# Optimization experiments

Hardware: AMD Instinct MI355X
Metric: run time of the kernel (lower is better)

## Reference

```python
import jax, jax.numpy as jnp
import numpy as np

B, C, H, W = 16, 512, 32, 32
COND_C, L_COND = 768, 77
N_GROUPS, N_HEADS = 8, 8
HEAD = C // N_HEADS
EPS = 1e-5


def setup_inputs() -> dict:
    key = jax.random.key(0)
    ks = jax.random.split(key, 6)
    s = lambda fan_in: 1.0 / np.sqrt(fan_in)
    return {
        "x_0": jax.random.normal(ks[0], (B, C, H, W), jnp.float32),
        "cond": jax.random.normal(ks[1], (B, L_COND, COND_C), jnp.float32),
        "gn_gamma": jnp.ones((C,), jnp.float32),
        "gn_beta": jnp.zeros((C,), jnp.float32),
        "qkv_w": jax.random.normal(ks[2], (3 * C, C), jnp.float32) * s(C),
        "qkv_b": jnp.zeros((3 * C,), jnp.float32),
        "cond_kv_w": jax.random.normal(ks[3], (2 * C, COND_C), jnp.float32) * s(COND_C),
        "cond_kv_b": jnp.zeros((2 * C,), jnp.float32),
        "out_w": jax.random.normal(ks[4], (C, C), jnp.float32) * s(C),
        "out_b": jnp.zeros((C,), jnp.float32),
    }


def reference(x_0, cond, gn_gamma, gn_beta, qkv_w, qkv_b, cond_kv_w, cond_kv_b, out_w, out_b):
    b, c, h, w = x_0.shape
    L = h * w
    # --- GroupNorm over (C/G, H, W) per group, per-channel affine ---
    xg = x_0.reshape(b, N_GROUPS, c // N_GROUPS, h * w)
    mu = xg.mean(axis=(2, 3), keepdims=True)
    var = xg.var(axis=(2, 3), keepdims=True)
    xn = ((xg - mu) * jax.lax.rsqrt(var + EPS)).reshape(b, c, h, w)
    xn = xn * gn_gamma[None, :, None, None] + gn_beta[None, :, None, None]
    # --- to tokens [B, L, C] ---
    x = xn.transpose(0, 2, 3, 1).reshape(b, L, c)
    # --- QKV ---
    qkv = x @ qkv_w.T + qkv_b  # [B, L, 3C]
    q, k, v = jnp.split(qkv, 3, axis=-1)
    q = q.reshape(b, L, N_HEADS, HEAD)
    k = k.reshape(b, L, N_HEADS, HEAD)
    v = v.reshape(b, L, N_HEADS, HEAD)
    # --- conditional K/V ---
    kv_c = cond @ cond_kv_w.T + cond_kv_b  # [B, Lc, 2C]
    k_c, v_c = jnp.split(kv_c, 2, axis=-1)
    Lc = cond.shape[1]
    k_c = k_c.reshape(b, Lc, N_HEADS, HEAD)
    v_c = v_c.reshape(b, Lc, N_HEADS, HEAD)
    K = jnp.concatenate([k, k_c], axis=1)  # [B, L+Lc, H, D]
    V = jnp.concatenate([v, v_c], axis=1)
    # --- attention (full score matrix, as in the original) ---
    scale = HEAD ** -0.5
    scores = jnp.einsum("bqhd,bkhd->bhqk", q, K) * scale
    att = jax.nn.softmax(scores, axis=-1)
    out = jnp.einsum("bhqk,bkhd->bqhd", att, V).reshape(b, L, c)
    out = out @ out_w.T + out_b
    # --- back to image + residual ---
    out = out.reshape(b, h, w, c).transpose(0, 3, 1, 2)
    return out + x_0
```

## Files before the change

### kernel.cpp

```cpp
#include <hip/hip_runtime.h>

typedef short bf16x8 __attribute__((ext_vector_type(8)));
typedef float f32x4 __attribute__((ext_vector_type(4)));
typedef float f32x16 __attribute__((ext_vector_type(16)));
typedef unsigned int u32x4 __attribute__((ext_vector_type(4)));

#define KVP 1152

__device__ __forceinline__ unsigned short f2b(float f) {
    unsigned int u = __float_as_uint(f);
    u += 0x7FFFu + ((u >> 16) & 1u);
    return (unsigned short)(u >> 16);
}

__device__ __forceinline__ f32x4 mfma16(bf16x8 a, bf16x8 b, f32x4 c) {
    return __builtin_amdgcn_mfma_f32_16x16x32_bf16(a, b, c, 0, 0, 0);
}
__device__ __forceinline__ f32x16 mfma32(bf16x8 a, bf16x8 b, f32x16 c) {
    return __builtin_amdgcn_mfma_f32_32x32x16_bf16(a, b, c, 0, 0, 0);
}
__device__ __forceinline__ float exp2_raw(float x) {
    float r; asm("v_exp_f32 %0, %1" : "=v"(r) : "v"(x)); return r;
}
__device__ __forceinline__ unsigned cvt_pk(float lo, float hi) {
    unsigned r; asm("v_cvt_pk_bf16_f32 %0, %1, %2" : "=v"(r) : "v"(lo), "v"(hi)); return r;
}

typedef __attribute__((address_space(3))) unsigned int lds_u32_t;
typedef const __attribute__((address_space(1))) unsigned int glb_u32_t;
__device__ __forceinline__ void async_cp16(const void* g, void* l) {
    __builtin_amdgcn_global_load_lds((glb_u32_t*)(unsigned long long)g,
                                     (lds_u32_t*)(unsigned int)(unsigned long long)l,
                                     16, 0, 0);
}

__global__ __launch_bounds__(256) void gn_part_k(const float* __restrict__ x, float2* __restrict__ part) {
    int blk = blockIdx.x;
    const float4* p = (const float4*)(x + (size_t)blk * 16384);
    float s = 0.f, ss = 0.f;
    for (int i = threadIdx.x; i < 4096; i += 256) {
        float4 v = p[i];
        s  += v.x + v.y + v.z + v.w;
        ss += v.x * v.x + v.y * v.y + v.z * v.z + v.w * v.w;
    }
#pragma unroll
    for (int o = 32; o; o >>= 1) { s += __shfl_down(s, o); ss += __shfl_down(ss, o); }
    __shared__ float red[8];
    int w = threadIdx.x >> 6;
    if ((threadIdx.x & 63) == 0) { red[w] = s; red[4 + w] = ss; }
    __syncthreads();
    if (threadIdx.x == 0) {
        s  = red[0] + red[1] + red[2] + red[3];
        ss = red[4] + red[5] + red[6] + red[7];
        part[blk] = make_float2(s, ss);
    }
}

__global__ __launch_bounds__(256) void gn_apply_k(const float* __restrict__ x, const float2* __restrict__ part,
                                                  const float* __restrict__ gamma, const float* __restrict__ beta,
                                                  unsigned short* __restrict__ xt) {
    int st = blockIdx.x & 15;
    int ct = (blockIdx.x >> 4) & 7;
    int b  = blockIdx.x >> 7;
    int bg = b * 8 + ct;
    float2 p0 = part[4 * bg], p1 = part[4 * bg + 1], p2 = part[4 * bg + 2], p3 = part[4 * bg + 3];
    float s = (p0.x + p1.x) + (p2.x + p3.x);
    float ss = (p0.y + p1.y) + (p2.y + p3.y);
    float mean = s * (1.f / 65536.f);
    float var  = ss * (1.f / 65536.f) - mean * mean;
    float rsig = rsqrtf(var + 1e-5f);
    __shared__ unsigned short tile[64][65];
    int tid = threadIdx.x;
#pragma unroll
    for (int it = 0; it < 4; ++it) {
        int idx = it * 256 + tid;
        int ci = idx >> 4, j4 = idx & 15;
        int c = ct * 64 + ci;
        float4 v = *(const float4*)(x + ((size_t)b * 512 + c) * 1024 + st * 64 + j4 * 4);
        float gs = gamma[c] * rsig;
        float bo = beta[c] - mean * gs;
        tile[j4 * 4 + 0][ci] = f2b(v.x * gs + bo);
        tile[j4 * 4 + 1][ci] = f2b(v.y * gs + bo);
        tile[j4 * 4 + 2][ci] = f2b(v.z * gs + bo);
        tile[j4 * 4 + 3][ci] = f2b(v.w * gs + bo);
    }
    __syncthreads();
#pragma unroll
    for (int it = 0; it < 4; ++it) {
        int idx = it * 256 + tid;
        int si = idx >> 4, q = idx & 15;
        uint2 u;
        u.x = (unsigned)tile[si][q * 4 + 0] | ((unsigned)tile[si][q * 4 + 1] << 16);
        u.y = (unsigned)tile[si][q * 4 + 2] | ((unsigned)tile[si][q * 4 + 3] << 16);
        *(uint2*)(xt + ((size_t)b * 1024 + st * 64 + si) * 512 + ct * 64 + q * 4) = u;
    }
}

__global__ __launch_bounds__(256) void cvt_k(const float* __restrict__ in, unsigned short* __restrict__ out, int n4) {
    int i = blockIdx.x * 256 + threadIdx.x;
    if (i < n4) {
        float4 v = ((const float4*)in)[i];
        uint2 u;
        u.x = (unsigned)f2b(v.x) | ((unsigned)f2b(v.y) << 16);
        u.y = (unsigned)f2b(v.z) | ((unsigned)f2b(v.w) << 16);
        ((uint2*)out)[i] = u;
    }
}

template <int EPI>
__global__ __launch_bounds__(256) void gemm128_k(const unsigned short* __restrict__ A,
                                                 const unsigned short* __restrict__ Bw,
                                                 const float* __restrict__ bias,
                                                 int K,
                                                 unsigned short* __restrict__ Qo,
                                                 unsigned short* __restrict__ Ko,
                                                 unsigned short* __restrict__ Vo,
                                                 const float* __restrict__ x0,
                                                 float* __restrict__ outp) {
    __shared__ __align__(16) unsigned short As[3][4096];
    __shared__ __align__(16) unsigned short Bs[3][4096];
    const int m0 = blockIdx.x * 128, n0 = blockIdx.y * 128;
    const int tid = threadIdx.x, lane = tid & 63, w = tid >> 6;
    const int wr = w >> 1, wc = w & 1;
    const int lc = lane & 15, lg = lane >> 4;

    const int sRow = lane >> 2;
    const int sSlot = (lane & 3) ^ ((lane >> 3) & 3);
    const unsigned short* aSrc0 = A + (size_t)(m0 + 16 * w + sRow) * K + sSlot * 8;
    const unsigned short* aSrc1 = A + (size_t)(m0 + 64 + 16 * w + sRow) * K + sSlot * 8;
    const unsigned short* bSrc0 = Bw + (size_t)(n0 + 16 * w + sRow) * K + sSlot * 8;
    const unsigned short* bSrc1 = Bw + (size_t)(n0 + 64 + 16 * w + sRow) * K + sSlot * 8;

    const int rSlot8 = (lg ^ ((lc >> 1) & 3)) * 8;

    f32x4 acc[4][4];
#pragma unroll
    for (int m = 0; m < 4; ++m)
#pragma unroll
        for (int n = 0; n < 4; ++n) acc[m][n] = (f32x4){0.f, 0.f, 0.f, 0.f};

    const int nT = K >> 5;
    async_cp16(aSrc0, &As[0][w * 512]);
    async_cp16(aSrc1, &As[0][(4 + w) * 512]);
    async_cp16(bSrc0, &Bs[0][w * 512]);
    async_cp16(bSrc1, &Bs[0][(4 + w) * 512]);
    async_cp16(aSrc0 + 32, &As[1][w * 512]);
    async_cp16(aSrc1 + 32, &As[1][(4 + w) * 512]);
    async_cp16(bSrc0 + 32, &Bs[1][w * 512]);
    async_cp16(bSrc1 + 32, &Bs[1][(4 + w) * 512]);

    int c = 0;
#pragma unroll 1
    for (int t = 0; t < nT; ++t) {
        if (t + 2 < nT) {
            int c2 = c + 2; if (c2 >= 3) c2 -= 3;
            const int k2 = (t + 2) << 5;
            async_cp16(aSrc0 + k2, &As[c2][w * 512]);
            async_cp16(aSrc1 + k2, &As[c2][(4 + w) * 512]);
            async_cp16(bSrc0 + k2, &Bs[c2][w * 512]);
            async_cp16(bSrc1 + k2, &Bs[c2][(4 + w) * 512]);
            asm volatile("s_waitcnt vmcnt(8)" ::: "memory");
        } else if (t + 1 < nT) {
            asm volatile("s_waitcnt vmcnt(4)" ::: "memory");
        } else {
            asm volatile("s_waitcnt vmcnt(0)" ::: "memory");
        }
        __builtin_amdgcn_s_barrier();

        bf16x8 af[4], bfr[4];
#pragma unroll
        for (int m = 0; m < 4; ++m)
            af[m] = *(const bf16x8*)&As[c][(wr * 64 + m * 16 + lc) * 32 + rSlot8];
#pragma unroll
        for (int n = 0; n < 4; ++n)
            bfr[n] = *(const bf16x8*)&Bs[c][(wc * 64 + n * 16 + lc) * 32 + rSlot8];
        asm volatile("s_waitcnt lgkmcnt(0)" ::: "memory");
        __builtin_amdgcn_sched_barrier(0);
        __builtin_amdgcn_s_barrier();

#pragma unroll
        for (int m = 0; m < 4; ++m)
#pragma unroll
            for (int n = 0; n < 4; ++n) {
                if (EPI == 0) acc[m][n] = mfma16(bfr[n], af[m], acc[m][n]);
                else          acc[m][n] = mfma16(af[m], bfr[n], acc[m][n]);
            }

        ++c; if (c == 3) c = 0;
    }

    if (EPI == 0) {
        const bool isQ = (n0 < 512);
        const float sc = isQ ? (0.125f * 1.44269504089f) : 1.f;
#pragma unroll
        for (int n = 0; n < 4; ++n) {
            const int c0 = n0 + wc * 64 + n * 16 + lg * 4;
            const float4 b4 = *(const float4*)&bias[c0];
#pragma unroll
            for (int m = 0; m < 4; ++m) {
                const int tok = m0 + wr * 64 + m * 16 + lc;
                const int b = tok >> 10, l = tok & 1023;
                float v0 = (acc[m][n][0] + b4.x) * sc;
                float v1 = (acc[m][n][1] + b4.y) * sc;
                float v2 = (acc[m][n][2] + b4.z) * sc;
                float v3 = (acc[m][n][3] + b4.w) * sc;
                uint2 u = make_uint2(cvt_pk(v0, v1), cvt_pk(v2, v3));
                if (isQ) {
                    const int hh = c0 >> 6, d = c0 & 63;
                    *(uint2*)(Qo + ((size_t)(b * 8 + hh) * 1024 + l) * 64 + d) = u;
                } else {
                    const int hh = (c0 - 512) >> 6, d = c0 & 63;
                    *(uint2*)(Ko + ((size_t)(b * 8 + hh) * KVP + l) * 64 + d) = u;
                }
            }
        }
    } else if (EPI == 1) {
#pragma unroll
        for (int n = 0; n < 4; ++n) {
            const int j = n0 + wc * 64 + n * 16 + lc;
            const int hh = j >> 6, d = j & 63;
            const float bv = bias[j];
#pragma unroll
            for (int m = 0; m < 4; ++m) {
                const int t0 = m0 + wr * 64 + m * 16 + lg * 4;
                const int b = t0 >> 10, l0 = t0 & 1023;
                uint2 u = make_uint2(cvt_pk(acc[m][n][0] + bv, acc[m][n][1] + bv),
                                     cvt_pk(acc[m][n][2] + bv, acc[m][n][3] + bv));
                *(uint2*)(Vo + ((size_t)(b * 8 + hh) * 64 + d) * KVP + l0) = u;
            }
        }
    } else {
#pragma unroll
        for (int n = 0; n < 4; ++n) {
            const int col = n0 + wc * 64 + n * 16 + lc;
            const float bv = bias[col];
#pragma unroll
            for (int m = 0; m < 4; ++m) {
                const int t0 = m0 + wr * 64 + m * 16 + lg * 4;
                const size_t a = ((size_t)(t0 >> 10) * 512 + col) * 1024 + (t0 & 1023);
                float4 xv = *(const float4*)(x0 + a);
                float4 o;
                o.x = acc[m][n][0] + bv + xv.x;
                o.y = acc[m][n][1] + bv + xv.y;
                o.z = acc[m][n][2] + bv + xv.z;
                o.w = acc[m][n][3] + bv + xv.w;
                *(float4*)(outp + a) = o;
            }
        }
    }
}

__global__ __launch_bounds__(256) void gemm_nt_k(const unsigned short* __restrict__ A,
                                                 const unsigned short* __restrict__ Bw,
                                                 const float* __restrict__ bias,
                                                 int M, int N, int K,
                                                 unsigned short* __restrict__ Ko,
                                                 unsigned short* __restrict__ Vo) {
    __shared__ unsigned short As[64][40];
    __shared__ unsigned short Bs[64][40];
    const int m0 = blockIdx.x * 64, n0 = blockIdx.y * 64;
    const int tid = threadIdx.x, lane = tid & 63, w = tid >> 6;
    const int lc = lane & 15, lg = lane >> 4;
    const int lrow = tid >> 2, lseg = tid & 3;
    f32x4 acc[4];
#pragma unroll
    for (int i = 0; i < 4; ++i) acc[i] = (f32x4){0.f, 0.f, 0.f, 0.f};

    for (int k0 = 0; k0 < K; k0 += 32) {
        uint4 av = make_uint4(0u, 0u, 0u, 0u);
        if (m0 + lrow < M) av = *(const uint4*)(A + (size_t)(m0 + lrow) * K + k0 + lseg * 8);
        *(uint4*)&As[lrow][lseg * 8] = av;
        uint4 bv = *(const uint4*)(Bw + (size_t)(n0 + lrow) * K + k0 + lseg * 8);
        *(uint4*)&Bs[lrow][lseg * 8] = bv;
        __syncthreads();
        bf16x8 af = *(const bf16x8*)&As[w * 16 + lc][lg * 8];
#pragma unroll
        for (int ct = 0; ct < 4; ++ct) {
            bf16x8 bfr = *(const bf16x8*)&Bs[ct * 16 + lc][lg * 8];
            acc[ct] = mfma16(af, bfr, acc[ct]);
        }
        __syncthreads();
    }

    const int rbase = m0 + w * 16 + lg * 4;
#pragma unroll
    for (int ct = 0; ct < 4; ++ct) {
        int col = n0 + ct * 16 + lc;
        float bv = bias[col];
#pragma unroll
        for (int r = 0; r < 4; ++r) {
            int token = rbase + r;
            if (token >= M) continue;
            float val = acc[ct][r] + bv;
            int b = token / 77, l = token - b * 77;
            if (col < 512) {
                int hh = col >> 6, d = col & 63;
                Ko[((size_t)(b * 8 + hh) * KVP + 1024 + l) * 64 + d] = f2b(val);
            } else {
                int j = col - 512, hh = j >> 6, d = j & 63;
                Vo[((size_t)(b * 8 + hh) * 64 + d) * KVP + 1024 + l] = f2b(val);
            }
        }
    }
}

__global__ __launch_bounds__(512) void attn2_k(const unsigned short* __restrict__ Q,
                                               const unsigned short* __restrict__ Kb,
                                               const unsigned short* __restrict__ Vt,
                                               unsigned short* __restrict__ atok) {
    __shared__ __align__(16) unsigned short lds[18432];

    const int bh = blockIdx.x >> 2;
    const int qt = blockIdx.x & 3;
    const int w  = threadIdx.x >> 6;
    const int lane = threadIdx.x & 63;
    const int ql = lane & 31, hi = lane >> 5;
    const int q0 = qt * 256 + w * 32;

    bf16x8 qf[4];
    const unsigned short* Qp = Q + ((size_t)bh * 1024 + q0 + ql) * 64 + hi * 8;
#pragma unroll
    for (int ks = 0; ks < 4; ++ks) qf[ks] = *(const bf16x8*)(Qp + ks * 16);

    const unsigned short* Kg = Kb + (size_t)bh * KVP * 64;
    const unsigned short* Vg = Vt + (size_t)bh * 64 * KVP;

    const int srow = lane >> 3;
    const int sc   = (((lane & 7) ^ (lane >> 3)) << 3);

    f32x16 o0, o1;
#pragma unroll
    for (int i = 0; i < 16; ++i) { o0[i] = 0.f; o1[i] = 0.f; }
    float mreg = -1e30f, lsum = 0.f;

    {
        uint4 kr = *(const uint4*)(Kg + (size_t)(8 * w + srow) * 64 + sc);
        uint4 vr = *(const uint4*)(Vg + (size_t)(8 * w + srow) * KVP + sc);
        *(uint4*)&lds[w * 512 + lane * 8] = kr;
        *(uint4*)&lds[4096 + w * 512 + lane * 8] = vr;
    }
    __syncthreads();

    int cur = 0;
    for (int it = 0; it < 18; ++it) {
        const int kv0 = it * 64;
        const bool pre = (it < 17);
        uint4 kn, vn;
        if (pre) {
            kn = *(const uint4*)(Kg + (size_t)(kv0 + 64 + 8 * w + srow) * 64 + sc);
            vn = *(const uint4*)(Vg + (size_t)(8 * w + srow) * KVP + kv0 + 64 + sc);
        }
        const int kb = cur * 8192, vb = cur * 8192 + 4096;

        f32x16 s0, s1;
#pragma unroll
        for (int i = 0; i < 16; ++i) { s0[i] = 0.f; s1[i] = 0.f; }
#pragma unroll
        for (int ks = 0; ks < 4; ++ks) {
            const int sl = ((ks * 2 + hi) ^ (ql & 7)) << 3;
            bf16x8 kf0 = *(const bf16x8*)&lds[kb + ql * 64 + sl];
            bf16x8 kf1 = *(const bf16x8*)&lds[kb + (32 + ql) * 64 + sl];
            s0 = mfma32(kf0, qf[ks], s0);
            s1 = mfma32(kf1, qf[ks], s1);
        }
        if (kv0 == 1088) {
#pragma unroll
            for (int r = 0; r < 16; ++r) {
                int kva = 1088 + (r & 3) + 8 * (r >> 2) + 4 * hi;
                if (kva >= 1101) s0[r] = -1e30f;
                if (kva + 32 >= 1101) s1[r] = -1e30f;
            }
        }

        float t[16];
#pragma unroll
        for (int i = 0; i < 16; ++i) t[i] = fmaxf(s0[i], s1[i]);
#pragma unroll
        for (int st = 8; st; st >>= 1)
#pragma unroll
            for (int i = 0; i < st; ++i) t[i] = fmaxf(t[i], t[i + st]);
        float pmax = fmaxf(t[0], __shfl_xor(t[0], 32));

        if (__any(pmax > mreg + 8.f)) {
            float mn = fmaxf(mreg, pmax);
            float al = exp2_raw(mreg - mn);
            mreg = mn;
            lsum *= al;
#pragma unroll
            for (int i = 0; i < 16; ++i) { o0[i] *= al; o1[i] *= al; }
        }

        unsigned pk0[8], pk1[8];
        float sA = 0.f, sB = 0.f, sC = 0.f, sD = 0.f;
#pragma unroll
        for (int i = 0; i < 8; ++i) {
            float a0 = exp2_raw(s0[2 * i] - mreg), a1 = exp2_raw(s0[2 * i + 1] - mreg);
            float b0 = exp2_raw(s1[2 * i] - mreg), b1 = exp2_raw(s1[2 * i + 1] - mreg);
            pk0[i] = cvt_pk(a0, a1);
            pk1[i] = cvt_pk(b0, b1);
            sA += a0; sB += a1; sC += b0; sD += b1;
        }
        float ls = (sA + sB) + (sC + sD);
        ls += __shfl_xor(ls, 32);
        lsum += ls;

#pragma unroll
        for (int t2 = 0; t2 < 2; ++t2) {
            const unsigned* pk = t2 ? pk1 : pk0;
#pragma unroll
            for (int v = 0; v < 2; ++v) {
                unsigned a0 = pk[4 * v], a1 = pk[4 * v + 1], a2 = pk[4 * v + 2], a3 = pk[4 * v + 3];
                unsigned x = __shfl_xor(hi ? a0 : a2, 32);
                unsigned y = __shfl_xor(hi ? a1 : a3, 32);
                u32x4 fw;
                fw.x = hi ? x : a0; fw.y = hi ? y : a1; fw.z = hi ? a2 : x; fw.w = hi ? a3 : y;
                bf16x8 pf = __builtin_bit_cast(bf16x8, fw);
                const int ks2 = 2 * t2 + v;
                const int sl = ((ks2 * 2 + hi) ^ (ql & 7)) << 3;
                bf16x8 vf0 = *(const bf16x8*)&lds[vb + ql * 64 + sl];
                bf16x8 vf1 = *(const bf16x8*)&lds[vb + (32 + ql) * 64 + sl];
                o0 = mfma32(vf0, pf, o0);
                o1 = mfma32(vf1, pf, o1);
            }
        }

        if (pre) {
            *(uint4*)&lds[(cur ^ 1) * 8192 + w * 512 + lane * 8] = kn;
            *(uint4*)&lds[(cur ^ 1) * 8192 + 4096 + w * 512 + lane * 8] = vn;
        }
        __syncthreads();
        cur ^= 1;
    }

    float rinv = 1.f / lsum;
    unsigned short* sw = &lds[w * 2304];
#pragma unroll
    for (int dt = 0; dt < 2; ++dt) {
#pragma unroll
        for (int rp = 0; rp < 8; ++rp) {
            float e0 = (dt ? o1[2 * rp] : o0[2 * rp]) * rinv;
            float e1 = (dt ? o1[2 * rp + 1] : o0[2 * rp + 1]) * rinv;
            int d = dt * 32 + ((2 * rp) & 3) + 8 * ((2 * rp) >> 2) + 4 * hi;
            *(unsigned*)&sw[ql * 72 + d] = cvt_pk(e0, e1);
        }
    }
    __syncthreads();
    {
        int i = threadIdx.x >> 1, hf = threadIdx.x & 1;
        const unsigned short* src = &lds[(i >> 5) * 2304 + (i & 31) * 72 + hf * 32];
        u32x4 r0 = *(const u32x4*)(src);
        u32x4 r1 = *(const u32x4*)(src + 8);
        u32x4 r2 = *(const u32x4*)(src + 16);
        u32x4 r3 = *(const u32x4*)(src + 24);
        int b = bh >> 3, h = bh & 7;
        unsigned short* gd = atok + ((size_t)b * 1024 + qt * 256 + i) * 512 + h * 64 + hf * 32;
        *(u32x4*)(gd) = r0;
        *(u32x4*)(gd + 8) = r1;
        *(u32x4*)(gd + 16) = r2;
        *(u32x4*)(gd + 24) = r3;
    }
}

extern "C" void kernel_launch(void* const* d_in, const int* in_sizes, int n_in,
                              void* d_out, int out_size, void* d_ws, size_t ws_size,
                              hipStream_t stream) {
    const float* x0     = (const float*)d_in[0];
    const float* cond   = (const float*)d_in[1];
    const float* gamma  = (const float*)d_in[2];
    const float* beta   = (const float*)d_in[3];
    const float* qkv_w  = (const float*)d_in[4];
    const float* qkv_b  = (const float*)d_in[5];
    const float* ckv_w  = (const float*)d_in[6];
    const float* ckv_b  = (const float*)d_in[7];
    const float* out_w  = (const float*)d_in[8];
    const float* out_b  = (const float*)d_in[9];
    float* outp = (float*)d_out;

    char* p = (char*)d_ws;
    float2* part = (float2*)p;           p += 4096;
    unsigned short* xt    = (unsigned short*)p; p += (size_t)16384 * 512 * 2;
    unsigned short* wqkv  = (unsigned short*)p; p += (size_t)1536 * 512 * 2;
    unsigned short* wckv  = (unsigned short*)p; p += (size_t)1024 * 768 * 2;
    unsigned short* wout  = (unsigned short*)p; p += (size_t)512 * 512 * 2;
    unsigned short* condb = (unsigned short*)p; p += (size_t)1232 * 768 * 2;
    unsigned short* Qb    = (unsigned short*)p; p += (size_t)16 * 8 * 1024 * 64 * 2;
    unsigned short* Kb    = (unsigned short*)p; p += (size_t)16 * 8 * KVP * 64 * 2;
    unsigned short* Vtb   = (unsigned short*)p; p += (size_t)16 * 8 * KVP * 64 * 2;
    unsigned short* atok  = (unsigned short*)p; p += (size_t)16384 * 512 * 2;

    gn_part_k<<<512, 256, 0, stream>>>(x0, part);
    gn_apply_k<<<2048, 256, 0, stream>>>(x0, part, gamma, beta, xt);
    cvt_k<<<768, 256, 0, stream>>>(qkv_w, wqkv, 196608);
    cvt_k<<<768, 256, 0, stream>>>(ckv_w, wckv, 196608);
    cvt_k<<<256, 256, 0, stream>>>(out_w, wout, 65536);
    cvt_k<<<924, 256, 0, stream>>>(cond, condb, 236544);

    gemm128_k<0><<<dim3(128, 8), 256, 0, stream>>>(xt, wqkv, qkv_b, 512,
                                                   Qb, Kb, nullptr, nullptr, nullptr);
    gemm128_k<1><<<dim3(128, 4), 256, 0, stream>>>(xt, wqkv + (size_t)1024 * 512, qkv_b + 1024, 512,
                                                   nullptr, nullptr, Vtb, nullptr, nullptr);
    gemm_nt_k<<<dim3(20, 16), 256, 0, stream>>>(condb, wckv, ckv_b, 1232, 1024, 768, Kb, Vtb);
    attn2_k<<<512, 512, 0, stream>>>(Qb, Kb, Vtb, atok);
    gemm128_k<2><<<dim3(128, 4), 256, 0, stream>>>(atok, wout, out_b, 512,
                                                   nullptr, nullptr, nullptr, x0, outp);
}
```

Measured before the change: 179.7 us.

## Merge weight conversions and QKV GEMMs, reorder attention blocks, add MFMA priority hints

```diff
diff --git a/kernel.cpp b/kernel.cpp
--- a/kernel.cpp
+++ b/kernel.cpp
@@ -25,6 +25,7 @@
 __device__ __forceinline__ unsigned cvt_pk(float lo, float hi) {
     unsigned r; asm("v_cvt_pk_bf16_f32 %0, %1, %2" : "=v"(r) : "v"(lo), "v"(hi)); return r;
 }
+__device__ __forceinline__ float f3(float a, float b, float c) { return fmaxf(fmaxf(a, b), c); }
 
 typedef __attribute__((address_space(3))) unsigned int lds_u32_t;
 typedef const __attribute__((address_space(1))) unsigned int glb_u32_t;
@@ -96,15 +97,20 @@
     }
 }
 
-__global__ __launch_bounds__(256) void cvt_k(const float* __restrict__ in, unsigned short* __restrict__ out, int n4) {
+__global__ __launch_bounds__(256) void cvtall_k(const float* __restrict__ a, unsigned short* __restrict__ oa,
+                                                const float* __restrict__ b, unsigned short* __restrict__ ob,
+                                                const float* __restrict__ c, unsigned short* __restrict__ oc,
+                                                const float* __restrict__ d, unsigned short* __restrict__ od) {
     int i = blockIdx.x * 256 + threadIdx.x;
-    if (i < n4) {
-        float4 v = ((const float4*)in)[i];
-        uint2 u;
-        u.x = (unsigned)f2b(v.x) | ((unsigned)f2b(v.y) << 16);
-        u.y = (unsigned)f2b(v.z) | ((unsigned)f2b(v.w) << 16);
-        ((uint2*)out)[i] = u;
-    }
+    const float* src; unsigned short* dst; int j;
+    if (i < 196608)      { src = a; dst = oa; j = i; }
+    else if (i < 393216) { src = b; dst = ob; j = i - 196608; }
+    else if (i < 458752) { src = c; dst = oc; j = i - 393216; }
+    else if (i < 695296) { src = d; dst = od; j = i - 458752; }
+    else return;
+    float4 v = ((const float4*)src)[j];
+    uint2 u = make_uint2(cvt_pk(v.x, v.y), cvt_pk(v.z, v.w));
+    ((uint2*)dst)[j] = u;
 }
 
 template <int EPI>
@@ -120,6 +126,7 @@
     __shared__ __align__(16) unsigned short As[3][4096];
     __shared__ __align__(16) unsigned short Bs[3][4096];
     const int m0 = blockIdx.x * 128, n0 = blockIdx.y * 128;
+    const bool swp = (EPI == 0) && (blockIdx.y < 8);
     const int tid = threadIdx.x, lane = tid & 63, w = tid >> 6;
     const int wr = w >> 1, wc = w & 1;
     const int lc = lane & 15, lg = lane >> 4;
@@ -178,55 +185,64 @@
         __builtin_amdgcn_sched_barrier(0);
         __builtin_amdgcn_s_barrier();
 
-#pragma unroll
-        for (int m = 0; m < 4; ++m)
+        if (swp) {
+#pragma unroll
+            for (int m = 0; m < 4; ++m)
+#pragma unroll
+                for (int n = 0; n < 4; ++n)
+                    acc[m][n] = mfma16(bfr[n], af[m], acc[m][n]);
+        } else {
+#pragma unroll
+            for (int m = 0; m < 4; ++m)
+#pragma unroll
+                for (int n = 0; n < 4; ++n)
+                    acc[m][n] = mfma16(af[m], bfr[n], acc[m][n]);
+        }
+
+        ++c; if (c == 3) c = 0;
+    }
+
+    if (EPI == 0) {
+        if (swp) {
+            const bool isQ = (n0 < 512);
+            const float sc = isQ ? (0.125f * 1.44269504089f) : 1.f;
 #pragma unroll
             for (int n = 0; n < 4; ++n) {
-                if (EPI == 0) acc[m][n] = mfma16(bfr[n], af[m], acc[m][n]);
-                else          acc[m][n] = mfma16(af[m], bfr[n], acc[m][n]);
-            }
-
-        ++c; if (c == 3) c = 0;
-    }
-
-    if (EPI == 0) {
-        const bool isQ = (n0 < 512);
-        const float sc = isQ ? (0.125f * 1.44269504089f) : 1.f;
-#pragma unroll
-        for (int n = 0; n < 4; ++n) {
-            const int c0 = n0 + wc * 64 + n * 16 + lg * 4;
-            const float4 b4 = *(const float4*)&bias[c0];
-#pragma unroll
-            for (int m = 0; m < 4; ++m) {
-                const int tok = m0 + wr * 64 + m * 16 + lc;
-                const int b = tok >> 10, l = tok & 1023;
-                float v0 = (acc[m][n][0] + b4.x) * sc;
-                float v1 = (acc[m][n][1] + b4.y) * sc;
-                float v2 = (acc[m][n][2] + b4.z) * sc;
-                float v3 = (acc[m][n][3] + b4.w) * sc;
-                uint2 u = make_uint2(cvt_pk(v0, v1), cvt_pk(v2, v3));
-                if (isQ) {
-                    const int hh = c0 >> 6, d = c0 & 63;
-                    *(uint2*)(Qo + ((size_t)(b * 8 + hh) * 1024 + l) * 64 + d) = u;
-                } else {
-                    const int hh = (c0 - 512) >> 6, d = c0 & 63;
-                    *(uint2*)(Ko + ((size_t)(b * 8 + hh) * KVP + l) * 64 + d) = u;
+                const int c0 = n0 + wc * 64 + n * 16 + lg * 4;
+                const float4 b4 = *(const float4*)&bias[c0];
+#pragma unroll
+                for (int m = 0; m < 4; ++m) {
+                    const int tok = m0 + wr * 64 + m * 16 + lc;
+                    const int b = tok >> 10, l = tok & 1023;
+                    float v0 = (acc[m][n][0] + b4.x) * sc;
+                    float v1 = (acc[m][n][1] + b4.y) * sc;
+                    float v2 = (acc[m][n][2] + b4.z) * sc;
+                    float v3 = (acc[m][n][3] + b4.w) * sc;
+                    uint2 u = make_uint2(cvt_pk(v0, v1), cvt_pk(v2, v3));
+                    if (isQ) {
+                        const int hh = c0 >> 6, d = c0 & 63;
+                        *(uint2*)(Qo + ((size_t)(b * 8 + hh) * 1024 + l) * 64 + d) = u;
+                    } else {
+                        const int hh = (c0 - 512) >> 6, d = c0 & 63;
+                        *(uint2*)(Ko + ((size_t)(b * 8 + hh) * KVP + l) * 64 + d) = u;
+                    }
                 }
             }
-        }
-    } else if (EPI == 1) {
-#pragma unroll
-        for (int n = 0; n < 4; ++n) {
-            const int j = n0 + wc * 64 + n * 16 + lc;
-            const int hh = j >> 6, d = j & 63;
-            const float bv = bias[j];
-#pragma unroll
-            for (int m = 0; m < 4; ++m) {
-                const int t0 = m0 + wr * 64 + m * 16 + lg * 4;
-                const int b = t0 >> 10, l0 = t0 & 1023;
-                uint2 u = make_uint2(cvt_pk(acc[m][n][0] + bv, acc[m][n][1] + bv),
-                                     cvt_pk(acc[m][n][2] + bv, acc[m][n][3] + bv));
-                *(uint2*)(Vo + ((size_t)(b * 8 + hh) * 64 + d) * KVP + l0) = u;
+        } else {
+#pragma unroll
+            for (int n = 0; n < 4; ++n) {
+                const int col = n0 + wc * 64 + n * 16 + lc;
+                const int j = col - 1024;
+                const int hh = j >> 6, d = j & 63;
+                const float bv = bias[col];
+#pragma unroll
+                for (int m = 0; m < 4; ++m) {
+                    const int t0 = m0 + wr * 64 + m * 16 + lg * 4;
+                    const int b = t0 >> 10, l0 = t0 & 1023;
+                    uint2 u = make_uint2(cvt_pk(acc[m][n][0] + bv, acc[m][n][1] + bv),
+                                         cvt_pk(acc[m][n][2] + bv, acc[m][n][3] + bv));
+                    *(uint2*)(Vo + ((size_t)(b * 8 + hh) * 64 + d) * KVP + l0) = u;
+                }
             }
         }
     } else {
@@ -310,8 +326,9 @@
                                                unsigned short* __restrict__ atok) {
     __shared__ __align__(16) unsigned short lds[18432];
 
-    const int bh = blockIdx.x >> 2;
-    const int qt = blockIdx.x & 3;
+    const int bid = blockIdx.x;
+    const int bh = bid & 127;
+    const int qt = bid >> 7;
     const int w  = threadIdx.x >> 6;
     const int lane = threadIdx.x & 63;
     const int ql = lane & 31, hi = lane >> 5;
@@ -355,6 +372,7 @@
         f32x16 s0, s1;
 #pragma unroll
         for (int i = 0; i < 16; ++i) { s0[i] = 0.f; s1[i] = 0.f; }
+        __builtin_amdgcn_s_setprio(1);
 #pragma unroll
         for (int ks = 0; ks < 4; ++ks) {
             const int sl = ((ks * 2 + hi) ^ (ql & 7)) << 3;
@@ -363,6 +381,7 @@
             s0 = mfma32(kf0, qf[ks], s0);
             s1 = mfma32(kf1, qf[ks], s1);
         }
+        __builtin_amdgcn_s_setprio(0);
         if (kv0 == 1088) {
 #pragma unroll
             for (int r = 0; r < 16; ++r) {
@@ -375,11 +394,11 @@
         float t[16];
 #pragma unroll
         for (int i = 0; i < 16; ++i) t[i] = fmaxf(s0[i], s1[i]);
-#pragma unroll
-        for (int st = 8; st; st >>= 1)
-#pragma unroll
-            for (int i = 0; i < st; ++i) t[i] = fmaxf(t[i], t[i + st]);
-        float pmax = fmaxf(t[0], __shfl_xor(t[0], 32));
+        float a0m = f3(t[0], t[1], t[2]),  a1m = f3(t[3], t[4], t[5]);
+        float a2m = f3(t[6], t[7], t[8]),  a3m = f3(t[9], t[10], t[11]);
+        float a4m = f3(t[12], t[13], t[14]);
+        float pm  = fmaxf(f3(a0m, a1m, a2m), f3(a3m, a4m, t[15]));
+        float pmax = fmaxf(pm, __shfl_xor(pm, 32));
 
         if (__any(pmax > mreg + 8.f)) {
             float mn = fmaxf(mreg, pmax);
@@ -419,8 +438,10 @@
                 const int sl = ((ks2 * 2 + hi) ^ (ql & 7)) << 3;
                 bf16x8 vf0 = *(const bf16x8*)&lds[vb + ql * 64 + sl];
                 bf16x8 vf1 = *(const bf16x8*)&lds[vb + (32 + ql) * 64 + sl];
+                __builtin_amdgcn_s_setprio(1);
                 o0 = mfma32(vf0, pf, o0);
                 o1 = mfma32(vf1, pf, o1);
+                __builtin_amdgcn_s_setprio(0);
             }
         }
 
@@ -490,15 +511,10 @@
 
     gn_part_k<<<512, 256, 0, stream>>>(x0, part);
     gn_apply_k<<<2048, 256, 0, stream>>>(x0, part, gamma, beta, xt);
-    cvt_k<<<768, 256, 0, stream>>>(qkv_w, wqkv, 196608);
-    cvt_k<<<768, 256, 0, stream>>>(ckv_w, wckv, 196608);
-    cvt_k<<<256, 256, 0, stream>>>(out_w, wout, 65536);
-    cvt_k<<<924, 256, 0, stream>>>(cond, condb, 236544);
-
-    gemm128_k<0><<<dim3(128, 8), 256, 0, stream>>>(xt, wqkv, qkv_b, 512,
-                                                   Qb, Kb, nullptr, nullptr, nullptr);
-    gemm128_k<1><<<dim3(128, 4), 256, 0, stream>>>(xt, wqkv + (size_t)1024 * 512, qkv_b + 1024, 512,
-                                                   nullptr, nullptr, Vtb, nullptr, nullptr);
+    cvtall_k<<<2716, 256, 0, stream>>>(qkv_w, wqkv, ckv_w, wckv, out_w, wout, cond, condb);
+
+    gemm128_k<0><<<dim3(128, 12), 256, 0, stream>>>(xt, wqkv, qkv_b, 512,
+                                                    Qb, Kb, Vtb, nullptr, nullptr);
     gemm_nt_k<<<dim3(20, 16), 256, 0, stream>>>(condb, wckv, ckv_b, 1232, 1024, 768, Kb, Vtb);
     attn2_k<<<512, 512, 0, stream>>>(Qb, Kb, Vtb, atok);
     gemm128_k<2><<<dim3(128, 4), 256, 0, stream>>>(atok, wout, out_b, 512,
```

Result: no change. 181.6 us (+1.0%).
